# Performance work log

Hardware: AMD Instinct MI355X
Metric: run time of the kernel (lower is better)

Reference implementation:

```python
import jax, jax.numpy as jnp
import numpy as np

B, C_IN, N_NODES = 512, 128, 511  # padded node axis = N_NODES + 1 (index 0 is the zero vector)


def setup_inputs() -> dict:
    key = jax.random.key(0)
    ks = jax.random.split(key, 8)
    trees = jax.random.normal(ks[0], (B, C_IN, N_NODES + 1), dtype=jnp.float32)
    idxes = jax.random.randint(ks[1], (B, 3 * N_NODES, 1), 0, N_NODES + 1, dtype=jnp.int64)

    def init_conv(k, out_c, in_c):
        kw, kb = jax.random.split(k)
        s = 1.0 / np.sqrt(in_c * 3)
        W = jax.random.uniform(kw, (out_c, in_c, 3), minval=-s, maxval=s, dtype=jnp.float32)
        b = jax.random.uniform(kb, (out_c,), minval=-s, maxval=s, dtype=jnp.float32)
        return W, b

    def init_lin(k, out_c, in_c):
        kw, kb = jax.random.split(k)
        s = 1.0 / np.sqrt(in_c)
        W = jax.random.uniform(kw, (out_c, in_c), minval=-s, maxval=s, dtype=jnp.float32)
        b = jax.random.uniform(kb, (out_c,), minval=-s, maxval=s, dtype=jnp.float32)
        return W, b

    W1, b1 = init_conv(ks[2], 256, C_IN)
    W2, b2 = init_conv(ks[3], 128, 256)
    W3, b3 = init_conv(ks[4], 64, 128)
    Wf1, bf1 = init_lin(ks[5], 32, 64)
    Wf2, bf2 = init_lin(ks[6], 1, 32)
    return dict(trees=trees, idxes=idxes, W1=W1, b1=b1, W2=W2, b2=b2,
                W3=W3, b3=b3, Wf1=Wf1, bf1=bf1, Wf2=Wf2, bf2=bf2)


def _tree_conv(x, idx, W, b):
    # x: [B, C, N+1], idx: [B, 3N] -> gather (self,left,right) triples, conv1d k=3 s=3
    Bs, C, _ = x.shape
    g = jnp.take_along_axis(x, jnp.broadcast_to(idx[:, None, :], (Bs, C, idx.shape[1])), axis=2)
    g = g.reshape(Bs, C, -1, 3)  # [B, C, N, 3]
    out = jnp.einsum('bcnk,ock->bon', g, W) + b[None, :, None]  # [B, O, N]
    zero = jnp.zeros((Bs, out.shape[1], 1), out.dtype)
    return jnp.concatenate([zero, out], axis=2)  # re-add zero-padding node at idx 0


def _tree_norm(x):
    # torch.std is unbiased (ddof=1); normalize over (channel, node) dims per tree
    mean = jnp.mean(x, axis=(1, 2), keepdims=True)
    n = x.shape[1] * x.shape[2]
    var = jnp.sum((x - mean) ** 2, axis=(1, 2), keepdims=True) / (n - 1)
    return (x - mean) / (jnp.sqrt(var) + 1e-5)


def _leaky(x):
    return jnp.where(x >= 0, x, 0.01 * x)


def reference(trees, idxes, W1, b1, W2, b2, W3, b3, Wf1, bf1, Wf2, bf2):
    idx = idxes[..., 0]  # [B, 3N]
    x = _leaky(_tree_norm(_tree_conv(trees, idx, W1, b1)))
    x = _leaky(_tree_norm(_tree_conv(x, idx, W2, b2)))
    x = _tree_norm(_tree_conv(x, idx, W3, b3))
    pooled = jnp.max(x, axis=2)  # DynamicPooling -> [B, 64]
    h = _leaky(pooled @ Wf1.T + bf1)
    return h @ Wf2.T + bf2  # [B, 1]
```

## Files before the change

kernel.cpp:

```cpp
#include <hip/hip_runtime.h>

#define TRIP 1533

typedef __attribute__((ext_vector_type(8))) short bf16x8;
typedef __attribute__((ext_vector_type(4))) float f32x4;

__device__ __forceinline__ void split2(float a, float b, unsigned& h, unsigned& l) {
    unsigned ba = __float_as_uint(a), bb = __float_as_uint(b);
    unsigned ha = ba & 0xFFFF0000u, hb = bb & 0xFFFF0000u;
    float ra = a - __uint_as_float(ha);
    float rb = b - __uint_as_float(hb);
    h = (ba >> 16) | hb;
    l = (__float_as_uint(ra) >> 16) | (__float_as_uint(rb) & 0xFFFF0000u);
}

template<int CIN, int COUT>
__global__ void k_repackW(const float* __restrict__ W,
                          unsigned short* __restrict__ Hi, unsigned short* __restrict__ Lo) {
    int id = blockIdx.x * 256 + threadIdx.x;
    if (id >= 3 * CIN * COUT) return;
    int o = id / (3 * CIN), kk = id % (3 * CIN);
    int ks = kk / CIN, c = kk % CIN;
    float v = W[(o * CIN + c) * 3 + ks];
    unsigned b = __float_as_uint(v);
    unsigned h = b & 0xFFFF0000u;
    float r = v - __uint_as_float(h);
    size_t dst = ((size_t)(kk >> 3) * COUT + o) * 8 + (kk & 7);
    Hi[dst] = (unsigned short)(b >> 16);
    Lo[dst] = (unsigned short)(__float_as_uint(r) >> 16);
}

__global__ void k_transpose(const float* __restrict__ in, float* __restrict__ out) {
    __shared__ float tl[64][129];
    int b = blockIdx.z, n0 = blockIdx.x * 64, t = threadIdx.x;
    int n = t & 63;
    for (int c = t >> 6; c < 128; c += 4)
        tl[n][c] = in[((size_t)b * 128 + c) * 512 + n0 + n];
    __syncthreads();
    int cq = t & 31;
    for (int nr = t >> 5; nr < 64; nr += 8) {
        float4 v = { tl[nr][cq*4+0], tl[nr][cq*4+1], tl[nr][cq*4+2], tl[nr][cq*4+3] };
        *(float4*)&out[((size_t)b * 512 + n0 + nr) * 128 + cq * 4] = v;
    }
}

__global__ void k_zero_row0(float* __restrict__ o1, float* __restrict__ o2, float* __restrict__ o3) {
    int b = blockIdx.x, t = threadIdx.x;
    if (t < 256) o1[(size_t)b * 512 * 256 + t] = 0.f;
    if (t < 128) o2[(size_t)b * 512 * 128 + t] = 0.f;
    if (t < 64)  o3[(size_t)b * 512 * 64  + t] = 0.f;
}

template<int CIN, int COUT, int OCH_T, bool NORM_IN>
__global__ __launch_bounds__(256, 3) void k_convmfma(
    const float* __restrict__ xin, const int* __restrict__ idx,
    const unsigned short* __restrict__ WHi, const unsigned short* __restrict__ WLo,
    const float* __restrict__ bias, float* __restrict__ out,
    const float* __restrict__ sIn, float* __restrict__ sOut)
{
    constexpr int K  = 3 * CIN;
    constexpr int NK = K / 32;
    constexpr int NI = OCH_T / 32;
    constexpr int OH = OCH_T / 2;
    constexpr int GP = 128 * 8 + 8;
    constexpr int GY = COUT / OCH_T;
    constexpr int P  = 4 * GY;
    constexpr int G8 = 8 * P;

    __shared__ unsigned short Gh[4 * GP], Gl[4 * GP];
    __shared__ float rs[4], rq[4];

    int b, bx, by;
    {
        const int gz = gridDim.z;
        int f = (blockIdx.z * GY + blockIdx.y) * 4 + blockIdx.x;
        if ((gz & 7) == 0) {
            int g = f / G8, w = f - g * G8;
            b = g * 8 + (w & 7);
            int blk = w >> 3;
            bx = blk & 3; by = blk >> 2;
        } else { b = blockIdx.z; bx = blockIdx.x; by = blockIdx.y; }
    }
    const int och0 = by * OCH_T;
    const int n0   = 1 + bx * 128;
    const int t    = threadIdx.x;
    const int lane = t & 63, wave = t >> 6;
    const int wm = wave >> 1, wn = wave & 1;
    const int l15 = lane & 15, l16 = lane >> 4;

    float mean = 0.f, inv = 1.f;
    if (NORM_IN) {
        float s = sIn[b * 2], ss = sIn[b * 2 + 1];
        const float nel = (float)(CIN * 512);
        float mu  = s / nel;
        float var = (ss - nel * mu * mu) / (nel - 1.f);
        mean = mu; inv = 1.f / (sqrtf(var) + 1e-5f);
    }

    const int nodeL = t & 127, ghalf = t >> 7, cb = ghalf * 16;
    int il0 = 0, il1 = 0, il2 = 0;
    if (n0 + nodeL <= 511) {
        const int* ip = &idx[b * TRIP + 3 * (n0 - 1 + nodeL)];
        il0 = ip[0]; il1 = ip[1]; il2 = ip[2];
    }
    const float* gBase = &xin[(size_t)b * 512 * CIN + cb];

    const unsigned short* wbH = WHi + ((size_t)l16 * COUT + och0 + wn * OH + l15) * 8;
    const unsigned short* wbL = WLo + ((size_t)l16 * COUT + och0 + wn * OH + l15) * 8;

    float4 g0, g1, g2, g3;
    auto loadG = [&](int ch) {
        int ks = (ch * 32) / CIN, c0 = (ch * 32) % CIN;
        int node = ks == 0 ? il0 : (ks == 1 ? il1 : il2);
        const float* s = gBase + (size_t)node * CIN + c0;
        g0 = *(const float4*)&s[0];  g1 = *(const float4*)&s[4];
        g2 = *(const float4*)&s[8];  g3 = *(const float4*)&s[12];
    };

    f32x4 acc[4][NI] = {};
    loadG(0);

    for (int ch = 0; ch < NK; ++ch) {
        __syncthreads();
        {
            float4 v0 = g0, v1 = g1, v2 = g2, v3 = g3;
            if (NORM_IN) {
                #define LKY(x) { x = (x - mean) * inv; x = x >= 0.f ? x : 0.01f * x; }
                LKY(v0.x) LKY(v0.y) LKY(v0.z) LKY(v0.w)
                LKY(v1.x) LKY(v1.y) LKY(v1.z) LKY(v1.w)
                LKY(v2.x) LKY(v2.y) LKY(v2.z) LKY(v2.w)
                LKY(v3.x) LKY(v3.y) LKY(v3.z) LKY(v3.w)
                #undef LKY
            }
            uint4 H0, L0, H1, L1;
            split2(v0.x, v0.y, H0.x, L0.x); split2(v0.z, v0.w, H0.y, L0.y);
            split2(v1.x, v1.y, H0.z, L0.z); split2(v1.z, v1.w, H0.w, L0.w);
            split2(v2.x, v2.y, H1.x, L1.x); split2(v2.z, v2.w, H1.y, L1.y);
            split2(v3.x, v3.y, H1.z, L1.z); split2(v3.z, v3.w, H1.w, L1.w);
            unsigned short* gh = &Gh[(2 * ghalf) * GP + nodeL * 8];
            unsigned short* gl = &Gl[(2 * ghalf) * GP + nodeL * 8];
            *(uint4*)gh = H0; *(uint4*)(gh + GP) = H1;
            *(uint4*)gl = L0; *(uint4*)(gl + GP) = L1;
        }
        if (ch + 1 < NK) loadG(ch + 1);
        bf16x8 Bh[NI], Bl[NI];
        {
            const size_t so = (size_t)(ch * 4) * COUT * 8;
            #pragma unroll
            for (int ni = 0; ni < NI; ++ni) {
                Bh[ni] = *(const bf16x8*)(wbH + so + ni * 128);
                Bl[ni] = *(const bf16x8*)(wbL + so + ni * 128);
            }
        }
        __syncthreads();

        bf16x8 Ah[4], Al[4];
        const unsigned short* ga = &Gh[l16 * GP + (wm * 64 + l15) * 8];
        const unsigned short* gb = &Gl[l16 * GP + (wm * 64 + l15) * 8];
        #pragma unroll
        for (int mi = 0; mi < 4; ++mi) {
            Ah[mi] = *(const bf16x8*)(ga + mi * 128);
            Al[mi] = *(const bf16x8*)(gb + mi * 128);
        }
        #pragma unroll
        for (int mi = 0; mi < 4; ++mi)
            #pragma unroll
            for (int ni = 0; ni < NI; ++ni) {
                acc[mi][ni] = __builtin_amdgcn_mfma_f32_16x16x32_bf16(Ah[mi], Bh[ni], acc[mi][ni], 0, 0, 0);
                acc[mi][ni] = __builtin_amdgcn_mfma_f32_16x16x32_bf16(Ah[mi], Bl[ni], acc[mi][ni], 0, 0, 0);
                acc[mi][ni] = __builtin_amdgcn_mfma_f32_16x16x32_bf16(Al[mi], Bh[ni], acc[mi][ni], 0, 0, 0);
            }
    }

    float lsum = 0.f, lss = 0.f;
    #pragma unroll
    for (int ni = 0; ni < NI; ++ni) {
        int ol = wn * OH + ni * 16 + l15;
        float bi = bias[och0 + ol];
        #pragma unroll
        for (int mi = 0; mi < 4; ++mi) {
            #pragma unroll
            for (int r = 0; r < 4; ++r) {
                int nl = wm * 64 + mi * 16 + l16 * 4 + r;
                int ng = n0 + nl;
                if (ng <= 511) {
                    float v = acc[mi][ni][r] + bi;
                    out[((size_t)b * 512 + ng) * COUT + och0 + ol] = v;
                    lsum += v; lss += v * v;
                }
            }
        }
    }

    #pragma unroll
    for (int off = 32; off > 0; off >>= 1) {
        lsum += __shfl_down(lsum, off);
        lss  += __shfl_down(lss, off);
    }
    if (lane == 0) { rs[wave] = lsum; rq[wave] = lss; }
    __syncthreads();
    if (t == 0) {
        atomicAdd(&sOut[b * 2],     rs[0] + rs[1] + rs[2] + rs[3]);
        atomicAdd(&sOut[b * 2 + 1], rq[0] + rq[1] + rq[2] + rq[3]);
    }
}

__global__ __launch_bounds__(256) void k_pool_fc(
    const float* __restrict__ x,
    const float* __restrict__ stats,
    const float* __restrict__ Wf1, const float* __restrict__ bf1,
    const float* __restrict__ Wf2, const float* __restrict__ bf2,
    float* __restrict__ outp)
{
    __shared__ float cm[4][64];
    __shared__ float pool[64];
    __shared__ float h[32];
    int b = blockIdx.x, t = threadIdx.x;
    int c = t & 63, g = t >> 6;
    float m = -1e30f;
    for (int n = 1 + g; n <= 511; n += 4)
        m = fmaxf(m, x[((size_t)b * 512 + n) * 64 + c]);
    cm[g][c] = m;
    __syncthreads();
    if (t < 64) {
        float mm = fmaxf(fmaxf(cm[0][t], cm[1][t]), fmaxf(cm[2][t], cm[3][t]));
        mm = fmaxf(mm, 0.f);
        float s = stats[b * 2], ss = stats[b * 2 + 1];
        const float nel = 64.f * 512.f;
        float mu  = s / nel;
        float var = (ss - nel * mu * mu) / (nel - 1.f);
        float inv = 1.f / (sqrtf(var) + 1e-5f);
        pool[t] = (mm - mu) * inv;
    }
    __syncthreads();
    if (t < 32) {
        float acc = bf1[t];
        for (int cc = 0; cc < 64; ++cc) acc += pool[cc] * Wf1[t * 64 + cc];
        h[t] = acc >= 0.f ? acc : 0.01f * acc;
    }
    __syncthreads();
    if (t == 0) {
        float acc = bf2[0];
        for (int j = 0; j < 32; ++j) acc += h[j] * Wf2[j];
        outp[b] = acc;
    }
}

extern "C" void kernel_launch(void* const* d_in, const int* in_sizes, int n_in,
                              void* d_out, int out_size, void* d_ws, size_t ws_size,
                              hipStream_t stream)
{
    const float* trees = (const float*)d_in[0];
    const int*   idx32 = (const int*)d_in[1];
    const float* W1  = (const float*)d_in[2];
    const float* b1  = (const float*)d_in[3];
    const float* W2  = (const float*)d_in[4];
    const float* b2  = (const float*)d_in[5];
    const float* W3  = (const float*)d_in[6];
    const float* b3  = (const float*)d_in[7];
    const float* Wf1 = (const float*)d_in[8];
    const float* bf1 = (const float*)d_in[9];
    const float* Wf2 = (const float*)d_in[10];
    const float* bf2 = (const float*)d_in[11];
    float* outp = (float*)d_out;
    char*  ws   = (char*)d_ws;

    float*          stats = (float*)ws;
    unsigned short* w1h = (unsigned short*)(ws + 12288);
    unsigned short* w1l = (unsigned short*)(ws + 208896);
    unsigned short* w2h = (unsigned short*)(ws + 405504);
    unsigned short* w2l = (unsigned short*)(ws + 602112);
    unsigned short* w3h = (unsigned short*)(ws + 798720);
    unsigned short* w3l = (unsigned short*)(ws + 847872);
    char* chunkBase = ws + 897024;
    float* s0 = stats, *s1 = stats + 1024, *s2 = stats + 2048;

    const size_t fixedB = 897024;
    int Bc = 512;
    while (Bc > 1 && fixedB + (size_t)Bc * 917504 > ws_size) Bc >>= 1;

    hipMemsetAsync(stats, 0, 12288, stream);
    k_repackW<128, 256><<<384, 256, 0, stream>>>(W1, w1h, w1l);
    k_repackW<256, 128><<<384, 256, 0, stream>>>(W2, w2h, w2l);
    k_repackW<128, 64><<<96, 256, 0, stream>>>(W3, w3h, w3l);

    float* t0   = (float*)chunkBase;
    float* out1 = (float*)(chunkBase + (size_t)Bc * 262144);
    float* out3 = (float*)(chunkBase + (size_t)Bc * 786432);

    for (int c0 = 0; c0 < 512; c0 += Bc) {
        const float* treesC = trees + (size_t)c0 * 128 * 512;
        const int*   idxC   = idx32 + (size_t)c0 * TRIP;

        k_transpose<<<dim3(8, 1, Bc), 256, 0, stream>>>(treesC, t0);
        k_convmfma<128, 256, 128, false><<<dim3(4, 2, Bc), 256, 0, stream>>>(
            t0, idxC, w1h, w1l, b1, out1, nullptr, s0 + c0 * 2);
        k_zero_row0<<<Bc, 256, 0, stream>>>(out1, t0, out3);
        k_convmfma<256, 128, 128, true><<<dim3(4, 1, Bc), 256, 0, stream>>>(
            out1, idxC, w2h, w2l, b2, t0, s0 + c0 * 2, s1 + c0 * 2);
        k_convmfma<128, 64, 64, true><<<dim3(4, 1, Bc), 256, 0, stream>>>(
            t0, idxC, w3h, w3l, b3, out3, s1 + c0 * 2, s2 + c0 * 2);
        k_pool_fc<<<Bc, 256, 0, stream>>>(out3, s2 + c0 * 2, Wf1, bf1, Wf2, bf2, outp + c0);
    }

    (void)in_sizes; (void)n_in; (void)out_size; (void)ws_size;
}
```

Baseline: 687.9 us.

## Double-buffer gathered tile in LDS with one barrier per K chunk

Doubles the LDS staging buffers and unrolls the K loop by two, alternating between buffers so each chunk needs one barrier instead of two. Two chunks of gathered inputs are prefetched in registers, letting global loads and LDS writes overlap the MFMA work on the other buffer. This costs twice the LDS and more registers, which may cut occupancy under launch_bounds(256,3). It assumes NK is even and relies on a hand-written s_waitcnt/s_barrier asm sequence for correctness.

New measurement: 875.6 us. 1.27x slower.

```diff
diff --git a/kernel.cpp b/kernel.cpp
--- a/kernel.cpp
+++ b/kernel.cpp
@@ -67,7 +67,7 @@
     constexpr int P  = 4 * GY;
     constexpr int G8 = 8 * P;
 
-    __shared__ unsigned short Gh[4 * GP], Gl[4 * GP];
+    __shared__ unsigned short Gh[8 * GP], Gl[8 * GP];
     __shared__ float rs[4], rq[4];
 
     int b, bx, by;
@@ -105,58 +105,51 @@
     }
     const float* gBase = &xin[(size_t)b * 512 * CIN + cb];
 
-    const unsigned short* wbH = WHi + ((size_t)l16 * COUT + och0 + wn * OH + l15) * 8;
-    const unsigned short* wbL = WLo + ((size_t)l16 * COUT + och0 + wn * OH + l15) * 8;
-
-    float4 g0, g1, g2, g3;
-    auto loadG = [&](int ch) {
+    auto loadG = [&](int ch, float4& g0, float4& g1, float4& g2, float4& g3) {
         int ks = (ch * 32) / CIN, c0 = (ch * 32) % CIN;
         int node = ks == 0 ? il0 : (ks == 1 ? il1 : il2);
         const float* s = gBase + (size_t)node * CIN + c0;
         g0 = *(const float4*)&s[0];  g1 = *(const float4*)&s[4];
         g2 = *(const float4*)&s[8];  g3 = *(const float4*)&s[12];
     };
+    auto stage = [&](int buf, float4 v0, float4 v1, float4 v2, float4 v3) {
+        if (NORM_IN) {
+            #define LKY(x) { x = (x - mean) * inv; x = x >= 0.f ? x : 0.01f * x; }
+            LKY(v0.x) LKY(v0.y) LKY(v0.z) LKY(v0.w)
+            LKY(v1.x) LKY(v1.y) LKY(v1.z) LKY(v1.w)
+            LKY(v2.x) LKY(v2.y) LKY(v2.z) LKY(v2.w)
+            LKY(v3.x) LKY(v3.y) LKY(v3.z) LKY(v3.w)
+            #undef LKY
+        }
+        uint4 H0, L0, H1, L1;
+        split2(v0.x, v0.y, H0.x, L0.x); split2(v0.z, v0.w, H0.y, L0.y);
+        split2(v1.x, v1.y, H0.z, L0.z); split2(v1.z, v1.w, H0.w, L0.w);
+        split2(v2.x, v2.y, H1.x, L1.x); split2(v2.z, v2.w, H1.y, L1.y);
+        split2(v3.x, v3.y, H1.z, L1.z); split2(v3.z, v3.w, H1.w, L1.w);
+        unsigned short* gh = &Gh[(buf * 4 + 2 * ghalf) * GP + nodeL * 8];
+        unsigned short* gl = &Gl[(buf * 4 + 2 * ghalf) * GP + nodeL * 8];
+        *(uint4*)gh = H0; *(uint4*)(gh + GP) = H1;
+        *(uint4*)gl = L0; *(uint4*)(gl + GP) = L1;
+    };
+
+    const unsigned short* wbH = WHi + ((size_t)l16 * COUT + och0 + wn * OH + l15) * 8;
+    const unsigned short* wbL = WLo + ((size_t)l16 * COUT + och0 + wn * OH + l15) * 8;
+
+    auto bload = [&](int ch, bf16x8* Bh, bf16x8* Bl) {
+        const size_t so = (size_t)(ch * 4) * COUT * 8;
+        #pragma unroll
+        for (int ni = 0; ni < NI; ++ni) {
+            Bh[ni] = *(const bf16x8*)(wbH + so + ni * 128);
+            Bl[ni] = *(const bf16x8*)(wbL + so + ni * 128);
+        }
+    };
 
     f32x4 acc[4][NI] = {};
-    loadG(0);
-
-    for (int ch = 0; ch < NK; ++ch) {
-        __syncthreads();
-        {
-            float4 v0 = g0, v1 = g1, v2 = g2, v3 = g3;
-            if (NORM_IN) {
-                #define LKY(x) { x = (x - mean) * inv; x = x >= 0.f ? x : 0.01f * x; }
-                LKY(v0.x) LKY(v0.y) LKY(v0.z) LKY(v0.w)
-                LKY(v1.x) LKY(v1.y) LKY(v1.z) LKY(v1.w)
-                LKY(v2.x) LKY(v2.y) LKY(v2.z) LKY(v2.w)
-                LKY(v3.x) LKY(v3.y) LKY(v3.z) LKY(v3.w)
-                #undef LKY
-            }
-            uint4 H0, L0, H1, L1;
-            split2(v0.x, v0.y, H0.x, L0.x); split2(v0.z, v0.w, H0.y, L0.y);
-            split2(v1.x, v1.y, H0.z, L0.z); split2(v1.z, v1.w, H0.w, L0.w);
-            split2(v2.x, v2.y, H1.x, L1.x); split2(v2.z, v2.w, H1.y, L1.y);
-            split2(v3.x, v3.y, H1.z, L1.z); split2(v3.z, v3.w, H1.w, L1.w);
-            unsigned short* gh = &Gh[(2 * ghalf) * GP + nodeL * 8];
-            unsigned short* gl = &Gl[(2 * ghalf) * GP + nodeL * 8];
-            *(uint4*)gh = H0; *(uint4*)(gh + GP) = H1;
-            *(uint4*)gl = L0; *(uint4*)(gl + GP) = L1;
-        }
-        if (ch + 1 < NK) loadG(ch + 1);
-        bf16x8 Bh[NI], Bl[NI];
-        {
-            const size_t so = (size_t)(ch * 4) * COUT * 8;
-            #pragma unroll
-            for (int ni = 0; ni < NI; ++ni) {
-                Bh[ni] = *(const bf16x8*)(wbH + so + ni * 128);
-                Bl[ni] = *(const bf16x8*)(wbL + so + ni * 128);
-            }
-        }
-        __syncthreads();
-
+
+    auto domfma = [&](int buf, bf16x8* Bh, bf16x8* Bl) {
         bf16x8 Ah[4], Al[4];
-        const unsigned short* ga = &Gh[l16 * GP + (wm * 64 + l15) * 8];
-        const unsigned short* gb = &Gl[l16 * GP + (wm * 64 + l15) * 8];
+        const unsigned short* ga = &Gh[(buf * 4 + l16) * GP + (wm * 64 + l15) * 8];
+        const unsigned short* gb = &Gl[(buf * 4 + l16) * GP + (wm * 64 + l15) * 8];
         #pragma unroll
         for (int mi = 0; mi < 4; ++mi) {
             Ah[mi] = *(const bf16x8*)(ga + mi * 128);
@@ -170,6 +163,26 @@
                 acc[mi][ni] = __builtin_amdgcn_mfma_f32_16x16x32_bf16(Ah[mi], Bl[ni], acc[mi][ni], 0, 0, 0);
                 acc[mi][ni] = __builtin_amdgcn_mfma_f32_16x16x32_bf16(Al[mi], Bh[ni], acc[mi][ni], 0, 0, 0);
             }
+    };
+
+    float4 A0, A1, A2, A3, B0, B1, B2, B3;
+    loadG(0, A0, A1, A2, A3);
+    loadG(1, B0, B1, B2, B3);
+
+    for (int ch = 0; ch < NK; ch += 2) {
+        stage(0, A0, A1, A2, A3);
+        bf16x8 Bh0[NI], Bl0[NI];
+        bload(ch, Bh0, Bl0);
+        if (ch + 2 < NK) loadG(ch + 2, A0, A1, A2, A3);
+        asm volatile("s_waitcnt lgkmcnt(0)\n\ts_barrier" ::: "memory");
+        domfma(0, Bh0, Bl0);
+
+        stage(1, B0, B1, B2, B3);
+        bf16x8 Bh1[NI], Bl1[NI];
+        bload(ch + 1, Bh1, Bl1);
+        if (ch + 3 < NK) loadG(ch + 3, B0, B1, B2, B3);
+        asm volatile("s_waitcnt lgkmcnt(0)\n\ts_barrier" ::: "memory");
+        domfma(1, Bh1, Bl1);
     }
 
     float lsum = 0.f, lss = 0.f;
```
